# Performance work log

Hardware: AMD Instinct MI355X
Metric: run time of the kernel (lower is better)

## Reference

```python
import jax, jax.numpy as jnp
import numpy as np

N_NODES = 15000
N_EDGES = 60000
NODE_VOCAB = 118 + 20000
EDGE_VOCAB = 4 + 50
NODE_INDIM = 64
EDGE_INDIM = 32
H = 32          # node_hidden_feats
EH = 64         # edge_hidden_feats
NUM_STEPS = 3   # num_step_message_passing
N_BOND_TYPES = 4  # edge ids < 4 are chemical bonds -> edge_func1, else knowledge relations -> edge_func2


def setup_inputs() -> dict:
    key = jax.random.key(0)
    ks = jax.random.split(key, 20)
    s = 0.05  # param scale for numerical stability
    return {
        "node_ids": jax.random.randint(ks[0], (N_NODES,), 0, NODE_VOCAB),
        "edge_ids": jax.random.randint(ks[1], (N_EDGES,), 0, EDGE_VOCAB),
        "src": jax.random.randint(ks[2], (N_EDGES,), 0, N_NODES),
        "dst": jax.random.randint(ks[3], (N_EDGES,), 0, N_NODES),
        "node_table": jax.random.normal(ks[4], (NODE_VOCAB, NODE_INDIM), jnp.float32),
        "edge_table": jax.random.normal(ks[5], (EDGE_VOCAB, EDGE_INDIM), jnp.float32),
        "proj_W": jax.random.normal(ks[6], (H, NODE_INDIM), jnp.float32) * s,
        "proj_b": jnp.zeros((H,), jnp.float32),
        "attn_w": jax.random.normal(ks[7], (2 * H,), jnp.float32) * s,
        "e1_W1": jax.random.normal(ks[8], (EH, EDGE_INDIM), jnp.float32) * s,
        "e1_b1": jnp.zeros((EH,), jnp.float32),
        "e1_W2": jax.random.normal(ks[9], (H * H, EH), jnp.float32) * s,
        "e1_b2": jnp.zeros((H * H,), jnp.float32),
        "e2_W1": jax.random.normal(ks[10], (EH, EDGE_INDIM), jnp.float32) * s,
        "e2_b1": jnp.zeros((EH,), jnp.float32),
        "e2_W2": jax.random.normal(ks[11], (H * H, EH), jnp.float32) * s,
        "e2_b2": jnp.zeros((H * H,), jnp.float32),
        "gru_Wih": jax.random.normal(ks[12], (3 * H, H), jnp.float32) * s,
        "gru_Whh": jax.random.normal(ks[13], (3 * H, H), jnp.float32) * s,
        "gru_bih": jnp.zeros((3 * H,), jnp.float32),
        "gru_bhh": jnp.zeros((3 * H,), jnp.float32),
    }


def _edge_softmax(logits, dst, num_nodes):
    # softmax over incoming edges of each destination node
    m = jax.ops.segment_max(logits, dst, num_segments=num_nodes)
    ex = jnp.exp(logits - m[dst])
    s = jax.ops.segment_sum(ex, dst, num_segments=num_nodes)
    return ex / s[dst]


def reference(node_ids, edge_ids, src, dst, node_table, edge_table, proj_W, proj_b,
              attn_w, e1_W1, e1_b1, e1_W2, e1_b2, e2_W1, e2_b1, e2_W2, e2_b2,
              gru_Wih, gru_Whh, gru_bih, gru_bhh):
    # --- embedding lookups ---
    nf = node_table[node_ids]                      # [N, node_indim]
    ef = edge_table[edge_ids]                      # [E, edge_indim]
    # --- project node feats: Linear + ReLU ---
    h = jax.nn.relu(nf @ proj_W.T + proj_b)        # [N, H]

    # --- per-edge weight matrices from the two edge MLPs (edge feats are
    # constant across message-passing steps, so compute once) ---
    def edge_mlp(W1, b1, W2, b2):
        z = jax.nn.relu(ef @ W1.T + b1)            # [E, EH]
        return (z @ W2.T + b2).reshape(-1, H, H)   # [E, H, H]

    W_e1 = edge_mlp(e1_W1, e1_b1, e1_W2, e1_b2)
    W_e2 = edge_mlp(e2_W1, e2_b1, e2_W2, e2_b2)
    is_bond = (edge_ids < N_BOND_TYPES)[:, None, None]
    W_edge = jnp.where(is_bond, W_e1, W_e2)        # [E, H, H]

    hidden = h                                     # GRU hidden state (seq of len 1 -> GRUCell)
    for _ in range(NUM_STEPS):
        # attention logits on edges: leaky_relu(attn_fc([h_src || h_dst]))
        a = jax.nn.leaky_relu(
            h[src] @ attn_w[:H] + h[dst] @ attn_w[H:])     # [E]
        alpha = _edge_softmax(a, dst, N_NODES)             # [E]
        # edge-conditioned message: (h_src @ W_e) weighted by attention
        msg = jnp.einsum('ei,eio->eo', h[src], W_edge) * alpha[:, None]  # [E, H]
        agg = jax.ops.segment_sum(msg, dst, num_segments=N_NODES)       # [N, H]
        m = jax.nn.relu(agg)
        # single GRU step (torch nn.GRU, 1 layer, seq_len 1)
        gi = m @ gru_Wih.T + gru_bih               # [N, 3H]
        gh = hidden @ gru_Whh.T + gru_bhh          # [N, 3H]
        ir, iz, inn = jnp.split(gi, 3, axis=1)
        hr, hz, hn = jnp.split(gh, 3, axis=1)
        r = jax.nn.sigmoid(ir + hr)
        z = jax.nn.sigmoid(iz + hz)
        n = jnp.tanh(inn + r * hn)
        hidden = (1.0 - z) * n + z * hidden
        h = hidden
    return h
```

## Files before the change

kernel.cpp:

```cpp
#include <hip/hip_runtime.h>
#include <math.h>

#define N_NODES   15000
#define N_EDGES   60000
#define EVOCAB    54
#define NODE_INDIM 64
#define EDGE_INDIM 32
#define H  32
#define EH 64
#define N_BOND 4

#define NPB   8
#define NBLK  (N_NODES / NPB)
#define CAP   128

#define TASK_VOCAB (EVOCAB * 1024)
#define TASK_PROJ  (N_NODES * H)
#define TASK_PACK  (H * H)
#define TASK_EDGE_BASE (TASK_VOCAB + TASK_PROJ + TASK_PACK)
#define TA_TOTAL   (TASK_EDGE_BASE + N_EDGES)

#define WT_OFF  0
#define H0_OFF  221184
#define H1_OFF  2141184
#define W4_OFF  4061184
#define W2_OFF  4077568
#define LS0_OFF 4085760
#define BS0_OFF 4145760
#define LS1_OFF 4205760
#define BS1_OFF 4265760
#define CNT_OFF 4325760
#define EPK_OFF 4333440

__global__ __launch_bounds__(256)
void setup_kernel(const int* __restrict__ node_ids, const int* __restrict__ src,
                  const int* __restrict__ dst, const int* __restrict__ eid,
                  const float* __restrict__ node_table, const float* __restrict__ edge_table,
                  const float* __restrict__ proj_W, const float* __restrict__ proj_b,
                  const float* __restrict__ attn_w,
                  const float* __restrict__ e1_W1, const float* __restrict__ e1_b1,
                  const float* __restrict__ e1_W2, const float* __restrict__ e1_b2,
                  const float* __restrict__ e2_W1, const float* __restrict__ e2_b1,
                  const float* __restrict__ e2_W2, const float* __restrict__ e2_b2,
                  const float* __restrict__ gWih, const float* __restrict__ gWhh,
                  float* __restrict__ Wt, float* __restrict__ h0,
                  float* __restrict__ ls, float* __restrict__ bs,
                  float4* __restrict__ Wpk4, float2* __restrict__ Wpk2,
                  int* __restrict__ cnt, int* __restrict__ blkE)
{
    int t = blockIdx.x * 256 + threadIdx.x;
    if (t >= TA_TOTAL) return;
    if (t < TASK_VOCAB) {
        int v = t >> 10, f = t & 1023, l = t & 63;
        const float* W1 = (v < N_BOND) ? e1_W1 : e2_W1;
        const float* b1 = (v < N_BOND) ? e1_b1 : e2_b1;
        const float* W2 = (v < N_BOND) ? e1_W2 : e2_W2;
        const float* b2 = (v < N_BOND) ? e1_b2 : e2_b2;
        const float4* ef4 = (const float4*)(edge_table + v * EDGE_INDIM);
        const float4* w14 = (const float4*)(W1 + l * EDGE_INDIM);
        float z = b1[l];
        #pragma unroll
        for (int j = 0; j < 8; ++j) {
            float4 a = ef4[j], b = w14[j];
            z += a.x*b.x + a.y*b.y + a.z*b.z + a.w*b.w;
        }
        z = fmaxf(z, 0.f);
        float y = b2[f];
        const float4* w24 = (const float4*)(W2 + f * EH);
        #pragma unroll
        for (int k = 0; k < 16; ++k) {
            float4 w = w24[k];
            y += __shfl(z, 4*k,   64) * w.x + __shfl(z, 4*k+1, 64) * w.y
               + __shfl(z, 4*k+2, 64) * w.z + __shfl(z, 4*k+3, 64) * w.w;
        }
        Wt[(v << 10) + f] = y;
    } else if (t < TASK_VOCAB + TASK_PROJ) {
        int q = t - TASK_VOCAB;
        int n = q >> 5, o = q & 31;
        int gid = node_ids[n];
        const float4* nf4 = (const float4*)(node_table + (size_t)gid * NODE_INDIM);
        const float4* wr4 = (const float4*)(proj_W + o * NODE_INDIM);
        float acc = proj_b[o];
        #pragma unroll
        for (int j = 0; j < 16; ++j) {
            float4 a = nf4[j], b = wr4[j];
            acc += a.x*b.x + a.y*b.y + a.z*b.z + a.w*b.w;
        }
        float hval = fmaxf(acc, 0.f);
        h0[q] = hval;
        float c1 = hval * attn_w[o], c2 = hval * attn_w[32 + o];
        #pragma unroll
        for (int k = 16; k > 0; k >>= 1) {
            c1 += __shfl_xor(c1, k, 32);
            c2 += __shfl_xor(c2, k, 32);
        }
        if (o == 0) { ls[n] = c1; bs[n] = c2; }
    } else if (t < TASK_EDGE_BASE) {
        int q = t - (TASK_VOCAB + TASK_PROJ);
        int j = q >> 5, o = q & 31;
        Wpk4[q] = make_float4(gWih[o * 32 + j], gWih[(32 + o) * 32 + j],
                              gWih[(64 + o) * 32 + j], gWhh[o * 32 + j]);
        Wpk2[q] = make_float2(gWhh[(32 + o) * 32 + j], gWhh[(64 + o) * 32 + j]);
    } else {
        int e = t - TASK_EDGE_BASE;
        int d = dst[e];
        int blk = d >> 3;
        int pack = src[e] | (eid[e] << 14) | ((d & 7) << 20);
        int slot = atomicAdd(&cnt[blk], 1);
        if (slot < CAP) blkE[blk * CAP + slot] = pack;
    }
}

__global__ __launch_bounds__(256)
void mp_kernel(const int* __restrict__ cnt, const int* __restrict__ blkE,
               const float* __restrict__ hc, const float* __restrict__ Wt,
               const float* __restrict__ attn_w,
               const float4* __restrict__ Wpk4, const float2* __restrict__ Wpk2,
               const float* __restrict__ gbih, const float* __restrict__ gbhh,
               const float* __restrict__ lsc, const float* __restrict__ bsc,
               float* __restrict__ lsn, float* __restrict__ bsn,
               float* __restrict__ op, int last)
{
    __shared__ float4 smsg4[CAP * 8];
    __shared__ float  sexs[CAP];
    __shared__ int    spk[CAP];
    __shared__ float  sbs[NPB];

    int b = blockIdx.x, tid = threadIdx.x;
    int cntB = cnt[b];
    if (cntB > CAP) cntB = CAP;
    if (tid < cntB) spk[tid] = blkE[b * CAP + tid];
    if (tid < NPB)  sbs[tid] = bsc[(b << 3) + tid];
    __syncthreads();

    int g = tid >> 5, o = tid & 31;

    for (int eb = 0; eb < cntB; eb += 16) {
        int e0 = eb + g, e1 = eb + 8 + g;
        float ex0 = 0.f; float4 p0 = make_float4(0.f, 0.f, 0.f, 0.f);
        if (e0 < cntB) {
            int pk = spk[e0];
            int sp = pk & 0x3FFF, vid = (pk >> 14) & 0x3F, dl = pk >> 20;
            float a = lsc[sp] + sbs[dl];
            a = (a > 0.f) ? a : 0.01f * a;
            ex0 = __expf(a);
            float hs = hc[(sp << 5) + o];
            const float4* W4 = (const float4*)(Wt + (vid << 10));
            #pragma unroll
            for (int k = 0; k < 8; ++k) {
                float4 w = W4[k * 32 + o];
                float hsk = __shfl(hs, 4 * k + (o >> 3), 32);
                p0.x += hsk * w.x; p0.y += hsk * w.y;
                p0.z += hsk * w.z; p0.w += hsk * w.w;
            }
        }
        float ex1 = 0.f; float4 p1 = make_float4(0.f, 0.f, 0.f, 0.f);
        if (e1 < cntB) {
            int pk = spk[e1];
            int sp = pk & 0x3FFF, vid = (pk >> 14) & 0x3F, dl = pk >> 20;
            float a = lsc[sp] + sbs[dl];
            a = (a > 0.f) ? a : 0.01f * a;
            ex1 = __expf(a);
            float hs = hc[(sp << 5) + o];
            const float4* W4 = (const float4*)(Wt + (vid << 10));
            #pragma unroll
            for (int k = 0; k < 8; ++k) {
                float4 w = W4[k * 32 + o];
                float hsk = __shfl(hs, 4 * k + (o >> 3), 32);
                p1.x += hsk * w.x; p1.y += hsk * w.y;
                p1.z += hsk * w.z; p1.w += hsk * w.w;
            }
        }
        p0.x += __shfl_xor(p0.x, 8, 32);  p0.y += __shfl_xor(p0.y, 8, 32);
        p0.z += __shfl_xor(p0.z, 8, 32);  p0.w += __shfl_xor(p0.w, 8, 32);
        p0.x += __shfl_xor(p0.x, 16, 32); p0.y += __shfl_xor(p0.y, 16, 32);
        p0.z += __shfl_xor(p0.z, 16, 32); p0.w += __shfl_xor(p0.w, 16, 32);
        p1.x += __shfl_xor(p1.x, 8, 32);  p1.y += __shfl_xor(p1.y, 8, 32);
        p1.z += __shfl_xor(p1.z, 8, 32);  p1.w += __shfl_xor(p1.w, 8, 32);
        p1.x += __shfl_xor(p1.x, 16, 32); p1.y += __shfl_xor(p1.y, 16, 32);
        p1.z += __shfl_xor(p1.z, 16, 32); p1.w += __shfl_xor(p1.w, 16, 32);
        if (e0 < cntB && o < 8) {
            smsg4[e0 * 8 + o] = make_float4(ex0 * p0.x, ex0 * p0.y, ex0 * p0.z, ex0 * p0.w);
            if (o == 0) sexs[e0] = ex0;
        }
        if (e1 < cntB && o < 8) {
            smsg4[e1 * 8 + o] = make_float4(ex1 * p1.x, ex1 * p1.y, ex1 * p1.z, ex1 * p1.w);
            if (o == 0) sexs[e1] = ex1;
        }
    }
    __syncthreads();

    const float* smsg = (const float*)smsg4;
    float sex = 0.f, acc = 0.f;
    for (int e = 0; e < cntB; ++e) {
        if ((spk[e] >> 20) == g) {
            acc += smsg[e * 32 + o];
            sex += sexs[e];
        }
    }
    float hv = hc[b * 256 + tid];
    float m = (sex != 0.f) ? fmaxf(acc / sex, 0.f) : 0.f;

    float gir = 0.f, giz = 0.f, gin = 0.f, ghr = 0.f, ghz = 0.f, ghn = 0.f;
    #pragma unroll 4
    for (int j = 0; j < 32; ++j) {
        float mj = __shfl(m, j, 32);
        float hj = __shfl(hv, j, 32);
        float4 a4 = Wpk4[j * 32 + o];
        float2 b2 = Wpk2[j * 32 + o];
        gir += mj * a4.x;  giz += mj * a4.y;  gin += mj * a4.z;
        ghr += hj * a4.w;  ghz += hj * b2.x;  ghn += hj * b2.y;
    }
    float r  = 1.f / (1.f + __expf(-(gir + gbih[o]      + ghr + gbhh[o])));
    float z  = 1.f / (1.f + __expf(-(giz + gbih[32 + o] + ghz + gbhh[32 + o])));
    float nn = tanhf(gin + gbih[64 + o] + r * (ghn + gbhh[64 + o]));
    float hid = (1.f - z) * nn + z * hv;
    op[b * 256 + tid] = hid;

    if (!last) {
        float c1 = hid * attn_w[o], c2 = hid * attn_w[32 + o];
        #pragma unroll
        for (int k = 16; k > 0; k >>= 1) {
            c1 += __shfl_xor(c1, k, 32);
            c2 += __shfl_xor(c2, k, 32);
        }
        if (o == 0) { lsn[(b << 3) + g] = c1; bsn[(b << 3) + g] = c2; }
    }
}

extern "C" void kernel_launch(void* const* d_in, const int* in_sizes, int n_in,
                              void* d_out, int out_size, void* d_ws, size_t ws_size,
                              hipStream_t stream) {
    const int*   node_ids   = (const int*)d_in[0];
    const int*   edge_ids   = (const int*)d_in[1];
    const int*   srcp       = (const int*)d_in[2];
    const int*   dstp       = (const int*)d_in[3];
    const float* node_table = (const float*)d_in[4];
    const float* edge_table = (const float*)d_in[5];
    const float* proj_W     = (const float*)d_in[6];
    const float* proj_b     = (const float*)d_in[7];
    const float* attn_w     = (const float*)d_in[8];
    const float* e1_W1 = (const float*)d_in[9];  const float* e1_b1 = (const float*)d_in[10];
    const float* e1_W2 = (const float*)d_in[11]; const float* e1_b2 = (const float*)d_in[12];
    const float* e2_W1 = (const float*)d_in[13]; const float* e2_b1 = (const float*)d_in[14];
    const float* e2_W2 = (const float*)d_in[15]; const float* e2_b2 = (const float*)d_in[16];
    const float* gWih  = (const float*)d_in[17]; const float* gWhh  = (const float*)d_in[18];
    const float* gbih  = (const float*)d_in[19]; const float* gbhh  = (const float*)d_in[20];
    float* outp = (float*)d_out;

    char* ws = (char*)d_ws;
    float*  Wt   = (float*)(ws + WT_OFF);
    float*  h0b  = (float*)(ws + H0_OFF);
    float*  h1b  = (float*)(ws + H1_OFF);
    float4* Wpk4 = (float4*)(ws + W4_OFF);
    float2* Wpk2 = (float2*)(ws + W2_OFF);
    float*  ls0  = (float*)(ws + LS0_OFF);
    float*  bs0  = (float*)(ws + BS0_OFF);
    float*  ls1  = (float*)(ws + LS1_OFF);
    float*  bs1  = (float*)(ws + BS1_OFF);
    int*    cnt  = (int*)  (ws + CNT_OFF);
    int*    blkE = (int*)  (ws + EPK_OFF);

    hipMemsetAsync(ws + CNT_OFF, 0, 7680, stream);

    setup_kernel<<<(TA_TOTAL + 255) / 256, 256, 0, stream>>>(
        node_ids, srcp, dstp, edge_ids, node_table, edge_table, proj_W, proj_b,
        attn_w, e1_W1, e1_b1, e1_W2, e1_b2, e2_W1, e2_b1, e2_W2, e2_b2,
        gWih, gWhh, Wt, h0b, ls0, bs0, Wpk4, Wpk2, cnt, blkE);

    float* hc = h0b;  float* hn = h1b;
    float* lc = ls0;  float* bc = bs0;
    float* ln = ls1;  float* bn = bs1;
    for (int step = 0; step < 3; ++step) {
        int last = (step == 2);
        float* op = last ? outp : hn;
        mp_kernel<<<NBLK, 256, 0, stream>>>(
            cnt, blkE, hc, Wt, attn_w, Wpk4, Wpk2, gbih, gbhh,
            lc, bc, ln, bn, op, last);
        float* tf;
        tf = hc; hc = hn; hn = tf;
        tf = lc; lc = ln; ln = tf;
        tf = bc; bc = bn; bn = tf;
    }
}
```

Baseline: 219.1 us.

## Pre-transpose edge-MLP and projection weights for coalesced setup reads

Adds a small pre-kernel that transposes the edge-MLP second-layer weights and the projection matrix, packs the GRU weights, and zeroes the bucket counters in place of the memset. In setup, the per-vocab MLP now reads the transposed W2 so adjacent threads load adjacent addresses, and the node projection loads each node row once and broadcasts its elements by shuffle instead of every lane reading a whole weight row. The aim is to replace strided per-thread row loads with coalesced loads, at the cost of one extra kernel launch and more shuffles.

```diff
diff --git a/kernel.cpp b/kernel.cpp
--- a/kernel.cpp
+++ b/kernel.cpp
@@ -16,46 +16,105 @@
 
 #define TASK_VOCAB (EVOCAB * 1024)
 #define TASK_PROJ  (N_NODES * H)
-#define TASK_PACK  (H * H)
-#define TASK_EDGE_BASE (TASK_VOCAB + TASK_PROJ + TASK_PACK)
+#define TASK_EDGE_BASE (TASK_VOCAB + TASK_PROJ)
 #define TA_TOTAL   (TASK_EDGE_BASE + N_EDGES)
 
-#define WT_OFF  0
-#define H0_OFF  221184
-#define H1_OFF  2141184
-#define W4_OFF  4061184
-#define W2_OFF  4077568
-#define LS0_OFF 4085760
-#define BS0_OFF 4145760
-#define LS1_OFF 4205760
-#define BS1_OFF 4265760
-#define CNT_OFF 4325760
-#define EPK_OFF 4333440
+#define WT_OFF   0
+#define H0_OFF   221184
+#define H1_OFF   2141184
+#define W4_OFF   4061184
+#define W2_OFF   4077568
+#define LS0_OFF  4085760
+#define BS0_OFF  4145760
+#define LS1_OFF  4205760
+#define BS1_OFF  4265760
+#define CNT_OFF  4325760
+#define EPK_OFF  4333440
+#define W2T1_OFF 5293440
+#define W2T2_OFF 5555584
+#define PT_OFF   5817728
+
+__global__ __launch_bounds__(256)
+void pre_kernel(const float* __restrict__ e1_W2, const float* __restrict__ e2_W2,
+                const float* __restrict__ proj_W,
+                const float* __restrict__ gWih, const float* __restrict__ gWhh,
+                float* __restrict__ W2T1, float* __restrict__ W2T2,
+                float* __restrict__ PT,
+                float4* __restrict__ Wpk4, float2* __restrict__ Wpk2,
+                int* __restrict__ cnt)
+{
+    int b = blockIdx.x, tid = threadIdx.x;
+    if (b < 32) {
+        __shared__ float st[64][65];
+        const float* in = (b < 16) ? e1_W2 : e2_W2;
+        float* out      = (b < 16) ? W2T1  : W2T2;
+        int f0 = (b & 15) * 64;
+        #pragma unroll
+        for (int it = 0; it < 16; ++it) {
+            int idx = it * 256 + tid;
+            int r = idx >> 6, c = idx & 63;
+            st[r][c] = in[(f0 + r) * 64 + c];
+        }
+        __syncthreads();
+        #pragma unroll
+        for (int it = 0; it < 16; ++it) {
+            int idx = it * 256 + tid;
+            int k = idx >> 6, f = idx & 63;
+            out[k * 1024 + f0 + f] = st[f][k];
+        }
+    } else if (b == 32) {
+        __shared__ float sp2[64][33];
+        #pragma unroll
+        for (int it = 0; it < 8; ++it) {
+            int idx = it * 256 + tid;
+            int o = idx >> 6, j = idx & 63;
+            sp2[j][o] = proj_W[idx];
+        }
+        __syncthreads();
+        #pragma unroll
+        for (int it = 0; it < 8; ++it) {
+            int idx = it * 256 + tid;
+            int j = idx >> 5, o = idx & 31;
+            PT[idx] = sp2[j][o];
+        }
+    } else if (b <= 36) {
+        int q = (b - 33) * 256 + tid;
+        int j = q >> 5, o = q & 31;
+        Wpk4[q] = make_float4(gWih[o * 32 + j], gWih[(32 + o) * 32 + j],
+                              gWih[(64 + o) * 32 + j], gWhh[o * 32 + j]);
+        Wpk2[q] = make_float2(gWhh[(32 + o) * 32 + j], gWhh[(64 + o) * 32 + j]);
+    } else {
+        #pragma unroll
+        for (int it = 0; it < 8; ++it) {
+            int idx = it * 256 + tid;
+            if (idx < NBLK) cnt[idx] = 0;
+        }
+    }
+}
 
 __global__ __launch_bounds__(256)
 void setup_kernel(const int* __restrict__ node_ids, const int* __restrict__ src,
                   const int* __restrict__ dst, const int* __restrict__ eid,
                   const float* __restrict__ node_table, const float* __restrict__ edge_table,
-                  const float* __restrict__ proj_W, const float* __restrict__ proj_b,
+                  const float* __restrict__ PT, const float* __restrict__ proj_b,
                   const float* __restrict__ attn_w,
                   const float* __restrict__ e1_W1, const float* __restrict__ e1_b1,
-                  const float* __restrict__ e1_W2, const float* __restrict__ e1_b2,
+                  const float* __restrict__ e1_b2,
                   const float* __restrict__ e2_W1, const float* __restrict__ e2_b1,
-                  const float* __restrict__ e2_W2, const float* __restrict__ e2_b2,
-                  const float* __restrict__ gWih, const float* __restrict__ gWhh,
+                  const float* __restrict__ e2_b2,
+                  const float* __restrict__ W2T1, const float* __restrict__ W2T2,
                   float* __restrict__ Wt, float* __restrict__ h0,
                   float* __restrict__ ls, float* __restrict__ bs,
-                  float4* __restrict__ Wpk4, float2* __restrict__ Wpk2,
                   int* __restrict__ cnt, int* __restrict__ blkE)
 {
     int t = blockIdx.x * 256 + threadIdx.x;
     if (t >= TA_TOTAL) return;
     if (t < TASK_VOCAB) {
         int v = t >> 10, f = t & 1023, l = t & 63;
-        const float* W1 = (v < N_BOND) ? e1_W1 : e2_W1;
-        const float* b1 = (v < N_BOND) ? e1_b1 : e2_b1;
-        const float* W2 = (v < N_BOND) ? e1_W2 : e2_W2;
-        const float* b2 = (v < N_BOND) ? e1_b2 : e2_b2;
+        const float* W1  = (v < N_BOND) ? e1_W1 : e2_W1;
+        const float* b1  = (v < N_BOND) ? e1_b1 : e2_b1;
+        const float* b2  = (v < N_BOND) ? e1_b2 : e2_b2;
+        const float* W2T = (v < N_BOND) ? W2T1  : W2T2;
         const float4* ef4 = (const float4*)(edge_table + v * EDGE_INDIM);
         const float4* w14 = (const float4*)(W1 + l * EDGE_INDIM);
         float z = b1[l];
@@ -66,26 +125,23 @@
         }
         z = fmaxf(z, 0.f);
         float y = b2[f];
-        const float4* w24 = (const float4*)(W2 + f * EH);
-        #pragma unroll
-        for (int k = 0; k < 16; ++k) {
-            float4 w = w24[k];
-            y += __shfl(z, 4*k,   64) * w.x + __shfl(z, 4*k+1, 64) * w.y
-               + __shfl(z, 4*k+2, 64) * w.z + __shfl(z, 4*k+3, 64) * w.w;
-        }
+        #pragma unroll 16
+        for (int k = 0; k < 64; ++k)
+            y += __shfl(z, k, 64) * W2T[k * 1024 + f];
         Wt[(v << 10) + f] = y;
-    } else if (t < TASK_VOCAB + TASK_PROJ) {
+    } else if (t < TASK_EDGE_BASE) {
         int q = t - TASK_VOCAB;
         int n = q >> 5, o = q & 31;
         int gid = node_ids[n];
-        const float4* nf4 = (const float4*)(node_table + (size_t)gid * NODE_INDIM);
-        const float4* wr4 = (const float4*)(proj_W + o * NODE_INDIM);
+        const float* nf = node_table + (size_t)gid * NODE_INDIM;
+        float nfa = nf[o], nfb = nf[32 + o];
         float acc = proj_b[o];
-        #pragma unroll
-        for (int j = 0; j < 16; ++j) {
-            float4 a = nf4[j], b = wr4[j];
-            acc += a.x*b.x + a.y*b.y + a.z*b.z + a.w*b.w;
-        }
+        #pragma unroll 8
+        for (int j = 0; j < 32; ++j)
+            acc += __shfl(nfa, j, 32) * PT[j * 32 + o];
+        #pragma unroll 8
+        for (int j = 0; j < 32; ++j)
+            acc += __shfl(nfb, j, 32) * PT[(32 + j) * 32 + o];
         float hval = fmaxf(acc, 0.f);
         h0[q] = hval;
         float c1 = hval * attn_w[o], c2 = hval * attn_w[32 + o];
@@ -95,12 +151,6 @@
             c2 += __shfl_xor(c2, k, 32);
         }
         if (o == 0) { ls[n] = c1; bs[n] = c2; }
-    } else if (t < TASK_EDGE_BASE) {
-        int q = t - (TASK_VOCAB + TASK_PROJ);
-        int j = q >> 5, o = q & 31;
-        Wpk4[q] = make_float4(gWih[o * 32 + j], gWih[(32 + o) * 32 + j],
-                              gWih[(64 + o) * 32 + j], gWhh[o * 32 + j]);
-        Wpk2[q] = make_float2(gWhh[(32 + o) * 32 + j], gWhh[(64 + o) * 32 + j]);
     } else {
         int e = t - TASK_EDGE_BASE;
         int d = dst[e];
@@ -260,13 +310,17 @@
     float*  bs1  = (float*)(ws + BS1_OFF);
     int*    cnt  = (int*)  (ws + CNT_OFF);
     int*    blkE = (int*)  (ws + EPK_OFF);
-
-    hipMemsetAsync(ws + CNT_OFF, 0, 7680, stream);
+    float*  W2T1 = (float*)(ws + W2T1_OFF);
+    float*  W2T2 = (float*)(ws + W2T2_OFF);
+    float*  PT   = (float*)(ws + PT_OFF);
+
+    pre_kernel<<<38, 256, 0, stream>>>(
+        e1_W2, e2_W2, proj_W, gWih, gWhh, W2T1, W2T2, PT, Wpk4, Wpk2, cnt);
 
     setup_kernel<<<(TA_TOTAL + 255) / 256, 256, 0, stream>>>(
-        node_ids, srcp, dstp, edge_ids, node_table, edge_table, proj_W, proj_b,
-        attn_w, e1_W1, e1_b1, e1_W2, e1_b2, e2_W1, e2_b1, e2_W2, e2_b2,
-        gWih, gWhh, Wt, h0b, ls0, bs0, Wpk4, Wpk2, cnt, blkE);
+        node_ids, srcp, dstp, edge_ids, node_table, edge_table, PT, proj_b,
+        attn_w, e1_W1, e1_b1, e1_b2, e2_W1, e2_b1, e2_b2, W2T1, W2T2,
+        Wt, h0b, ls0, bs0, cnt, blkE);
 
     float* hc = h0b;  float* hn = h1b;
     float* lc = ls0;  float* bc = bs0;
```

Measured after the change: 209.8 us. 4.3% less time.
